# Kernel tuning notes

Hardware: AMD Instinct MI355X
Metric: run time of the kernel (lower is better)

The kernel has to match this reference:

```python
import jax, jax.numpy as jnp
import numpy as np

WINDOW = 512
STEP = WINDOW // 2


def hamming_window(n):
    # torch.hamming_window default is periodic=True: 0.54 - 0.46*cos(2*pi*k/n)
    return (0.54 - 0.46 * jnp.cos(2.0 * jnp.pi * jnp.arange(n) / n)).astype(jnp.float32)


def fft_convolve(a, b):
    # ortho-normalized rfft spectra, irfft, crop back to n samples.
    n = a.shape[-1]
    pa = jnp.pad(a, [(0, 0)] * (a.ndim - 1) + [(0, n)])
    pb = jnp.pad(b, [(0, 0)] * (b.ndim - 1) + [(0, n)])
    spec = jnp.fft.rfft(pa, axis=-1, norm='ortho') * jnp.fft.rfft(pb, axis=-1, norm='ortho')
    return jnp.fft.irfft(spec, n=2 * n, axis=-1, norm='ortho')[..., :n]


def fft_shift(a, shift):
    # repo's fft_shift: fractional shift via phase ramp in rfft domain of the
    n = a.shape[-1]
    shift_samples = shift * n * 0.5  # [..., 1]
    pa = jnp.pad(a, [(0, 0)] * (a.ndim - 1) + [(0, n)])
    spec = jnp.fft.rfft(pa, axis=-1, norm='ortho')  # [..., n+1]
    n_coeffs = spec.shape[-1]
    ramp = (jnp.arange(n_coeffs) * 2j * jnp.pi) / n_coeffs
    phase = jnp.exp(-ramp * shift_samples)  # broadcast over last dim
    return jnp.fft.irfft(spec * phase, n=2 * n, axis=-1, norm='ortho')


def setup_inputs() -> dict:
    key = jax.random.key(0)
    k1, k2 = jax.random.split(key)
    B, n = 4, 32768
    recon = jax.random.normal(k1, (B, 1, n), dtype=jnp.float32)
    target = jax.random.normal(k2, (B, 1, n), dtype=jnp.float32)
    return {"recon": recon, "target": target}


def reference(recon, target):
    batch = recon.shape[0]
    n_samples = recon.shape[-1]
    n_frames = (n_samples - WINDOW) // STEP + 1  # unfold(-1, 512, 256)

    # unfold: gather overlapping frames [B, n_frames, WINDOW]
    idx = jnp.arange(n_frames)[:, None] * STEP + jnp.arange(WINDOW)[None, :]
    frames = recon[:, 0, :][:, idx]  # [B, n_frames, WINDOW]
    windowed = (frames * hamming_window(WINDOW))[:, None, :, :]  # [B,1,F,W]

    # zero-pad each frame up to n_samples (the torch.cat with zeros)
    windowed = jnp.pad(windowed, ((0, 0), (0, 0), (0, 0), (0, n_samples - WINDOW)))

    # FFT cross-correlation surrogate against the full target
    fm = fft_convolve(windowed, target[:, :, None, :])[..., :n_samples]  # [B,1,F,n]

    positions = jnp.argmax(fm, axis=-1, keepdims=True).astype(jnp.float32) / n_samples

    positioned = fft_shift(windowed, positions)[..., :n_samples]  # [B,1,F,n]
    positioned = jnp.sum(positioned, axis=2).reshape(batch, 1, n_samples)

    return jnp.mean((positioned - target) ** 2)
```

## Files before the change

kernel.cpp:

```cpp
#include <hip/hip_runtime.h>
#include <math.h>

#define N_SAMP   32768
#define WINDOW   512
#define STEP     256
#define NFRAMES  127
#define NB       4
#define RTRUNC   1280
#define NSLAB    32
#define BPAD     776
#define HW       3104

#define WS_WF   0
#define WS_WFH  260096
#define WS_WFL  391168
#define WS_PV   522240
#define WS_M    587776
#define WS_CNT  588288
#define WS_LIST 588304
#define WS_H    592400
#define WS_PART 2169232

typedef _Float16 f16x8 __attribute__((ext_vector_type(8)));
typedef float f32x16 __attribute__((ext_vector_type(16)));

#define SW(L) ((L) ^ (((L) >> 3) & 7))

#define FMA4(A, LO, HI)                                           \
    A.x = fmaf(c.x, HI.x, A.x); A.x = fmaf(c.y, LO.w, A.x);       \
    A.x = fmaf(c.z, LO.z, A.x); A.x = fmaf(c.w, LO.y, A.x);       \
    A.y = fmaf(c.x, HI.y, A.y); A.y = fmaf(c.y, HI.x, A.y);       \
    A.y = fmaf(c.z, LO.w, A.y); A.y = fmaf(c.w, LO.z, A.y);       \
    A.z = fmaf(c.x, HI.z, A.z); A.z = fmaf(c.y, HI.y, A.z);       \
    A.z = fmaf(c.z, HI.x, A.z); A.z = fmaf(c.w, LO.w, A.z);       \
    A.w = fmaf(c.x, HI.w, A.w); A.w = fmaf(c.y, HI.z, A.w);       \
    A.w = fmaf(c.z, HI.y, A.w); A.w = fmaf(c.w, HI.x, A.w);

__global__ __launch_bounds__(256) void k_wf(const float* __restrict__ recon,
                                            float* __restrict__ wf,
                                            _Float16* __restrict__ wfh) {
    int e = blockIdx.x * 256 + threadIdx.x;
    int w     = e & 511;
    int bf128 = e >> 9;
    int f = bf128 & 127;
    int b = bf128 >> 7;
    float val = 0.f;
    if (f < NFRAMES) {
        float ham = 0.54f - 0.46f * (float)cos((double)w * (M_PI / 256.0));
        val = ham * recon[b * N_SAMP + f * STEP + w];
        wf[(b * NFRAMES + f) * 512 + w] = val;
    }
    size_t tr = (((size_t)b * 64 + (w >> 3)) * 128 + f) * 8 + (w & 7);
    wfh[tr] = (_Float16)val;
}

__global__ __launch_bounds__(256, 4) void k_argmax_mfma(
        const float* __restrict__ tgt,
        const _Float16* __restrict__ wfh,
        float* __restrict__ pv) {
    __shared__ _Float16 sbh[8 * BPAD];
    const int tid   = threadIdx.x;
    const int chunk = blockIdx.x & 127;
    const int half  = (blockIdx.x >> 7) & 1;
    const int b     = blockIdx.x >> 8;
    const int T0    = chunk * 256;
    const int TB    = T0 + 255;
    const float* tb = tgt + b * N_SAMP;

    for (int oc = tid; oc < 768; oc += 256) {
        int r = oc / 96, s = oc - r * 96;
        int base = TB - r - 8 * s;
        _Float16 h8[8];
#pragma unroll
        for (int j = 0; j < 8; ++j) {
            int t = base - j;
            h8[j] = (_Float16)((t >= 0) ? tb[t] : 0.0f);
        }
        *(f16x8*)&sbh[r * BPAD + 8 * s] = *(f16x8*)h8;
    }
    __syncthreads();

    const int wv  = tid >> 6;
    const int q   = (tid >> 5) & 1;
    const int cl  = tid & 31;
    const int nt0 = 2 * wv;
    const int rp  = 7 - (cl & 7);
    const _Float16* Ah0 = wfh + ((size_t)b * 64) * 1024 + (half * 64 + cl) * 8;

    f32x16 acc00 = (f32x16)(0.f);
    f32x16 acc01 = (f32x16)(0.f);
    f32x16 acc10 = (f32x16)(0.f);
    f32x16 acc11 = (f32x16)(0.f);

    int off = q * 1024;
    int ea  = rp * BPAD + (255 - 32 * nt0 - cl + 8 * q - rp);
    f16x8 a0  = *(const f16x8*)(Ah0 + off);
    f16x8 a1  = *(const f16x8*)(Ah0 + off + 256);
    f16x8 bh0 = *(const f16x8*)&sbh[ea];
    f16x8 bh1 = *(const f16x8*)&sbh[ea - 32];
#pragma unroll
    for (int k0 = 0; k0 < 512; k0 += 16) {
        f16x8 a0n  = *(const f16x8*)(Ah0 + off + 2048);
        f16x8 a1n  = *(const f16x8*)(Ah0 + off + 2304);
        f16x8 bh0n = *(const f16x8*)&sbh[ea + 16];
        f16x8 bh1n = *(const f16x8*)&sbh[ea - 16];
        acc00 = __builtin_amdgcn_mfma_f32_32x32x16_f16(a0, bh0, acc00, 0, 0, 0);
        acc01 = __builtin_amdgcn_mfma_f32_32x32x16_f16(a0, bh1, acc01, 0, 0, 0);
        acc10 = __builtin_amdgcn_mfma_f32_32x32x16_f16(a1, bh0, acc10, 0, 0, 0);
        acc11 = __builtin_amdgcn_mfma_f32_32x32x16_f16(a1, bh1, acc11, 0, 0, 0);
        a0 = a0n; a1 = a1n; bh0 = bh0n; bh1 = bh1n;
        off += 2048; ea += 16;
    }

    __syncthreads();
    float* sval = (float*)sbh;
#pragma unroll
    for (int r = 0; r < 16; ++r) {
        float v0 = fmaxf(acc00[r], acc01[r]);
        float v1 = fmaxf(acc10[r], acc11[r]);
#pragma unroll
        for (int mm = 1; mm <= 16; mm <<= 1) {
            v0 = fmaxf(v0, __shfl_xor(v0, mm));
            v1 = fmaxf(v1, __shfl_xor(v1, mm));
        }
        if (cl == 0) {
            int row = (r & 3) + 8 * (r >> 2) + 4 * q;
            sval[row * 4 + wv]        = v0;
            sval[(32 + row) * 4 + wv] = v1;
        }
    }
    __syncthreads();
    if (tid < 64) {
        float v = fmaxf(fmaxf(sval[tid * 4], sval[tid * 4 + 1]),
                        fmaxf(sval[tid * 4 + 2], sval[tid * 4 + 3]));
        pv[((size_t)b * 128 + half * 64 + tid) * 128 + chunk] = v;
    }
}

__global__ __launch_bounds__(256) void k_vmax(const float* __restrict__ tgt,
                                              const float* __restrict__ wf,
                                              const float* __restrict__ pv,
                                              int* __restrict__ marr) {
    __shared__ float wfr[512];
    __shared__ float tg[768];
    __shared__ float rv[256];
    __shared__ int   ri[256];
    __shared__ int   clist[32];
    __shared__ int   ccnt;
    const int tid = threadIdx.x;
    const int fr  = blockIdx.x;
    const int b   = fr / NFRAMES;
    const int f   = fr - b * NFRAMES;
    const float* prow = pv + ((size_t)b * 128 + f) * 128;
    const float* tb   = tgt + b * N_SAMP;

    for (int i = tid; i < 512; i += 256) wfr[i] = wf[(size_t)fr * 512 + i];

    float mv = (tid < 128) ? prow[tid] : -3.4e38f;
    rv[tid] = mv;
    __syncthreads();
    for (int s = 128; s > 0; s >>= 1) {
        if (tid < s) rv[tid] = fmaxf(rv[tid], rv[tid + s]);
        __syncthreads();
    }
    float m0 = rv[0];
    if (tid == 0) ccnt = 0;
    __syncthreads();
    float eps = 0.012f * fabsf(m0) + 1e-3f;
    if (tid < 128 && mv >= m0 - eps) {
        int k = atomicAdd(&ccnt, 1);
        if (k < 32) clist[k] = tid;
    }
    __syncthreads();
    int nc = ccnt;
    int total = (nc <= 32) ? nc : 128;
    float bestv = -3.4e38f; int bestt = 0x7fffffff;
    for (int ci = 0; ci < total; ++ci) {
        int c = (nc <= 32) ? clist[ci] : ci;
        int T0 = c * 256;
        __syncthreads();
        for (int y = tid; y < 768; y += 256) {
            int t = T0 - 511 + y;
            tg[y] = (t >= 0 && t < N_SAMP) ? tb[t] : 0.0f;
        }
        __syncthreads();
        float a = 0.f;
        for (int w2 = 0; w2 < 512; ++w2)
            a = fmaf(wfr[w2], tg[511 + tid - w2], a);
        int tt = T0 + tid;
        if (a > bestv || (a == bestv && tt < bestt)) { bestv = a; bestt = tt; }
    }
    rv[tid] = bestv; ri[tid] = bestt;
    __syncthreads();
    for (int s = 128; s > 0; s >>= 1) {
        if (tid < s) {
            float v2 = rv[tid + s]; int i2 = ri[tid + s];
            if (v2 > rv[tid] || (v2 == rv[tid] && i2 < ri[tid])) {
                rv[tid] = v2; ri[tid] = i2;
            }
        }
        __syncthreads();
    }
    if (tid == 0) marr[fr] = ri[0];
}

__global__ __launch_bounds__(256) void k_coef(const int* __restrict__ marr,
                                              float* __restrict__ hbuf) {
    const int bf  = blockIdx.x;
    const int tid = threadIdx.x;
    const double invD = 1.0 / 2147549184.0;
    const float  sd   = 4.7936899603827e-05f;
    const float  trf  = (float)(RTRUNC + 4) / 65536.0f;
    int m = marr[bf];
    int p = (int)rint((double)m * (32768.0 / 32769.0));
    int jlo = p - (RTRUNC + 8); if (jlo < -512) jlo = -512; jlo &= ~3;
    float* hr = hbuf + (size_t)bf * HW;
    if (m == 0) {
        for (int k4 = tid; k4 < 776; k4 += 256) {
            int j0 = jlo + 4 * k4;
            float4 vq = make_float4((j0 == 0) ? 1.0f : 0.0f, 0.f, 0.f, 0.f);
            *(float4*)(hr + 4 * k4) = vq;
        }
        return;
    }
    double md32768 = (double)m * 32768.0;
    double sp = sin((double)m * (M_PI / 32769.0));
    float Cp = (float)(sp * (1.0 / 65536.0));
    if (m & 1) Cp = -Cp;
    float Cn = -Cp;
    for (int k4 = tid; k4 < 776; k4 += 256) {
        int j0 = jlo + 4 * k4;
        double A0 = (double)j0 * 32769.0 - md32768;
        double rA0 = A0 * invD;
        float f0v = (float)(rA0 - rint(rA0));
        float4 vq;
        if (fabsf(f0v) > trf) {
            vq = make_float4(0.f, 0.f, 0.f, 0.f);
        } else if (fabsf(f0v) < 6.2e-5f) {
#pragma unroll
            for (int k = 0; k < 4; ++k) {
                double rA = (A0 + (double)k * 32769.0) * invD;
                float ff = (float)(rA - rint(rA));
                float r2;
                if (ff == 0.0f) r2 = 65535.0f;
                else {
                    float s, c2;
                    __sincosf((float)M_PI * ff, &s, &c2);
                    r2 = c2 * __builtin_amdgcn_rcpf(s);
                }
                ((float*)&vq)[k] = ((k & 1) ? Cn : Cp) * r2;
            }
        } else {
            float s, c2;
            __sincosf((float)M_PI * f0v, &s, &c2);
            vq.x = Cp * (c2 * __builtin_amdgcn_rcpf(s));
            float s1 = fmaf(c2, sd, s);
            float c1 = fmaf(-s, sd, c2);
            vq.y = Cn * (c1 * __builtin_amdgcn_rcpf(s1));
            float s2 = fmaf(c1, sd, s1);
            float cc2 = fmaf(-s1, sd, c1);
            vq.z = Cp * (cc2 * __builtin_amdgcn_rcpf(s2));
            float s3 = fmaf(cc2, sd, s2);
            float c3 = fmaf(-s2, sd, cc2);
            vq.w = Cn * (c3 * __builtin_amdgcn_rcpf(s3));
        }
        *(float4*)(hr + 4 * k4) = vq;
    }
}

__global__ __launch_bounds__(256) void k_sched(const int* __restrict__ marr,
                                               int* __restrict__ list,
                                               int* __restrict__ cnt,
                                               int nslab) {
    __shared__ int scnt[64];
    __shared__ int total;
    const int tid = threadIdx.x;
    if (tid < 64) scnt[tid] = 0;
    if (tid == 0) total = 0;
    __syncthreads();
    const int RT8 = RTRUNC + 8;
    for (int bf = tid; bf < NB * NFRAMES; bf += 256) {
        int b = bf / NFRAMES;
        int m = marr[bf];
        int p = (int)rint((double)m * (32768.0 / 32769.0));
        int lo = p - RT8;        if (lo < 0) lo = 0;
        int hi = p + RT8 + 511;  if (hi > N_SAMP - 1) hi = N_SAMP - 1;
        int r0 = lo >> 11, r1 = hi >> 11;
        for (int r = r0; r <= r1; ++r) {
            int bc = (b << 4) | r;
            int s = atomicAdd(&scnt[bc], 1);
            int k = atomicAdd(&total, 1);
            list[k] = (bf << 16) | (r << 8) | s;
        }
    }
    __syncthreads();
    int n = total;
    for (int k = tid; k < n; k += 256) {
        int v = list[k];
        int bf = (v >> 16) & 0x3fff;
        int r = (v >> 8) & 15;
        int b = bf / NFRAMES;
        if (scnt[(b << 4) | r] > nslab) list[k] = v | (1 << 30);
    }
    if (tid == 0) {
        int mx = 0;
        for (int i = 0; i < 64; ++i) mx = (scnt[i] > mx) ? scnt[i] : mx;
        cnt[0] = n;
        cnt[1] = (mx > nslab) ? nslab : mx;
    }
}

#define LDBLK2(nn) (*(const float4*)(s_h + 4 * SW(Lt + (nn))))
#define CB3(g, A, Bq, Cq)                                         \
    {                                                             \
        float4 tnew = LDBLK2(126 - (g));                          \
        const float4 c = wc[(g)];                                 \
        FMA4(acc0, w[A], w[Bq]); FMA4(acc1, w[Bq], w[Cq]);        \
        w[Cq] = tnew;                                             \
    }
#define CB3_NL(g, A, Bq, Cq)                                      \
    {                                                             \
        const float4 c = wc[(g)];                                 \
        FMA4(acc0, w[A], w[Bq]); FMA4(acc1, w[Bq], w[Cq]);        \
    }

__global__ __launch_bounds__(256, 8) void k_shift_acc(const float* __restrict__ wf,
                                                      const int* __restrict__ marr,
                                                      const int* __restrict__ list,
                                                      const int* __restrict__ cnt,
                                                      const float* __restrict__ hbuf,
                                                      float* __restrict__ part,
                                                      int slabmask) {
    __shared__ __align__(16) float s_h[2560];
    const int tid = threadIdx.x;
    const int Lt  = 2 * tid;
    const int Ltw = (tid >> 6) * 128;
    const int n   = cnt[0];

    for (int se = blockIdx.x; se < n; se += gridDim.x) {
        int v     = list[se];
        int bf    = (v >> 16) & 0x3fff;
        int r     = (v >> 8) & 15;
        int slot  = v & 255;
        int isat  = (v >> 30) & 1;
        int b     = bf / NFRAMES;
        int t0s   = r << 11;
        const float4* __restrict__ wc = (const float4*)(wf + bf * 512);

        int m  = marr[bf];
        int pr = (int)rint((double)m * (32768.0 / 32769.0));
        int jlo = pr - (RTRUNC + 8); if (jlo < -512) jlo = -512; jlo &= ~3;
        int kb0 = ((t0s - 512) - jlo) >> 2;
        const float4* __restrict__ hb = (const float4*)(hbuf + (size_t)bf * HW);

        __syncthreads();
        for (int e4 = tid; e4 < 640; e4 += 256) {
            int kb = kb0 + e4;
            float4 vq = (kb >= 0 && kb < 776) ? hb[kb]
                                              : make_float4(0.f, 0.f, 0.f, 0.f);
            *(float4*)(s_h + 4 * SW(e4)) = vq;
        }
        __syncthreads();

        int blo = (pr - (RTRUNC + 8) - (t0s - 512)) >> 2;
        int bhi = (pr + (RTRUNC + 8) - (t0s - 512)) >> 2;
        if (blo < 0) blo = 0;
        if (bhi > 639) bhi = 639;

        float4 acc0 = make_float4(0.f, 0.f, 0.f, 0.f);
        float4 acc1 = acc0;

        int gmin = Ltw + 127 - bhi; if (gmin < 0) gmin = 0;
        int gmax = Ltw + 255 - blo; if (gmax > 127) gmax = 127;
        if (gmin <= gmax) {
            int go0 = gmin / 3;
            bool tail = (gmax >= 126);
            int goE = tail ? 42 : (gmax / 3 + 1);
            int gb0 = 3 * go0;
            float4 w[3];
            w[0] = LDBLK2(127 - gb0);
            w[1] = LDBLK2(128 - gb0);
            w[2] = LDBLK2(129 - gb0);
            for (int go = go0; go < goE && go < 42; ++go) {
                const int gb = 3 * go;
                CB3(gb + 0, 0, 1, 2);
                CB3(gb + 1, 2, 0, 1);
                CB3(gb + 2, 1, 2, 0);
            }
            if (tail) { CB3(126, 0, 1, 2); CB3_NL(127, 2, 0, 1); }
        }

        int slab = slot & slabmask;
        float* ob = part + (size_t)slab * (NB * N_SAMP) + b * N_SAMP + t0s;
        if (!isat) {
            *(float4*)(ob + 8 * tid)     = acc0;
            *(float4*)(ob + 8 * tid + 4) = acc1;
        } else {
            float* p0 = ob + 8 * tid;
            atomicAdd(p0 + 0, acc0.x); atomicAdd(p0 + 1, acc0.y);
            atomicAdd(p0 + 2, acc0.z); atomicAdd(p0 + 3, acc0.w);
            atomicAdd(p0 + 4, acc1.x); atomicAdd(p0 + 5, acc1.y);
            atomicAdd(p0 + 6, acc1.z); atomicAdd(p0 + 7, acc1.w);
        }
    }
}

__global__ __launch_bounds__(256) void k_mse(const float* __restrict__ part,
                                             const float* __restrict__ tgt,
                                             float* __restrict__ out,
                                             const int* __restrict__ cnt,
                                             int nslab) {
    __shared__ float sred[4];
    int e = blockIdx.x * 256 + threadIdx.x;
    int ng = cnt[1];
    if (ng > nslab) ng = nslab;
    float s0 = 0.f, s1 = 0.f, s2 = 0.f, s3 = 0.f;
    int g = 0;
    for (; g + 4 <= ng; g += 4) {
        s0 += part[(size_t)(g + 0) * (NB * N_SAMP) + e];
        s1 += part[(size_t)(g + 1) * (NB * N_SAMP) + e];
        s2 += part[(size_t)(g + 2) * (NB * N_SAMP) + e];
        s3 += part[(size_t)(g + 3) * (NB * N_SAMP) + e];
    }
    for (; g < ng; ++g)
        s0 += part[(size_t)g * (NB * N_SAMP) + e];
    float s = (s0 + s1) + (s2 + s3);
    float d = s - tgt[e];
    float v = d * d;
#pragma unroll
    for (int off = 32; off > 0; off >>= 1) v += __shfl_down(v, off, 64);
    int lane = threadIdx.x & 63, wid = threadIdx.x >> 6;
    if (lane == 0) sred[wid] = v;
    __syncthreads();
    if (threadIdx.x == 0) {
        float sm = sred[0] + sred[1] + sred[2] + sred[3];
        atomicAdd(out, sm * (1.0f / 131072.0f));
    }
}

extern "C" void kernel_launch(void* const* d_in, const int* in_sizes, int n_in,
                              void* d_out, int out_size, void* d_ws, size_t ws_size,
                              hipStream_t stream) {
    const float* recon = (const float*)d_in[0];
    const float* tgt   = (const float*)d_in[1];
    float* out = (float*)d_out;
    float* W   = (float*)d_ws;

    float*     wf   = W + WS_WF;
    _Float16*  wfh  = (_Float16*)(W + WS_WFH);
    float*     pv   = W + WS_PV;
    int*       marr = (int*)(W + WS_M);
    int*       cnt  = (int*)(W + WS_CNT);
    int*       list = (int*)(W + WS_LIST);
    float*     hbuf = W + WS_H;
    float*     part = W + WS_PART;

    int nslab = NSLAB;
    while (nslab > 1 &&
           ((size_t)WS_PART + (size_t)nslab * NB * N_SAMP) * sizeof(float) > ws_size)
        nslab >>= 1;

    hipMemsetAsync(out, 0, sizeof(float), stream);
    hipMemsetAsync(part, 0, (size_t)nslab * NB * N_SAMP * sizeof(float), stream);

    k_wf<<<1024, 256, 0, stream>>>(recon, wf, wfh);
    k_argmax_mfma<<<1024, 256, 0, stream>>>(tgt, wfh, pv);
    k_vmax<<<NB * NFRAMES, 256, 0, stream>>>(tgt, wf, pv, marr);
    k_coef<<<NB * NFRAMES, 256, 0, stream>>>(marr, hbuf);
    k_sched<<<1, 256, 0, stream>>>(marr, list, cnt, nslab);
    k_shift_acc<<<2048, 256, 0, stream>>>(wf, marr, list, cnt, hbuf, part, nslab - 1);
    k_mse<<<512, 256, 0, stream>>>(part, tgt, out, cnt, nslab);
}
```

Before: 181.0 us.

## Split shift-accumulate work items in half and give each thread four outputs

Each scheduled 2048-sample segment becomes two 1024-sample half-segments, so every block handles half as much output and each thread produces four outputs instead of eight. The shared-memory staging buffer shrinks to match. The inner loop is rewritten as a two-step sliding window over float4 taps with a single accumulator, and the grid is doubled. The aim is more parallelism and occupancy with a smaller LDS footprint. The cost is that the coefficient and staging loads are repeated for each half, and each thread has less reuse of its loaded values.

```diff
diff --git a/kernel.cpp b/kernel.cpp
--- a/kernel.cpp
+++ b/kernel.cpp
@@ -310,19 +310,7 @@
     }
 }
 
-#define LDBLK2(nn) (*(const float4*)(s_h + 4 * SW(Lt + (nn))))
-#define CB3(g, A, Bq, Cq)                                         \
-    {                                                             \
-        float4 tnew = LDBLK2(126 - (g));                          \
-        const float4 c = wc[(g)];                                 \
-        FMA4(acc0, w[A], w[Bq]); FMA4(acc1, w[Bq], w[Cq]);        \
-        w[Cq] = tnew;                                             \
-    }
-#define CB3_NL(g, A, Bq, Cq)                                      \
-    {                                                             \
-        const float4 c = wc[(g)];                                 \
-        FMA4(acc0, w[A], w[Bq]); FMA4(acc1, w[Bq], w[Cq]);        \
-    }
+#define LDB(nn) (*(const float4*)(s_h + 4 * SW((nn) + 4)))
 
 __global__ __launch_bounds__(256, 8) void k_shift_acc(const float* __restrict__ wf,
                                                       const int* __restrict__ marr,
@@ -331,76 +319,72 @@
                                                       const float* __restrict__ hbuf,
                                                       float* __restrict__ part,
                                                       int slabmask) {
-    __shared__ __align__(16) float s_h[2560];
+    __shared__ __align__(16) float s_h[4 * 392];
     const int tid = threadIdx.x;
-    const int Lt  = 2 * tid;
-    const int Ltw = (tid >> 6) * 128;
-    const int n   = cnt[0];
-
-    for (int se = blockIdx.x; se < n; se += gridDim.x) {
-        int v     = list[se];
+    const int Lh  = tid;
+    const int W0  = tid & ~63;
+    const int n2  = 2 * cnt[0];
+
+    for (int se = blockIdx.x; se < n2; se += gridDim.x) {
+        int v     = list[se >> 1];
+        int hh    = se & 1;
         int bf    = (v >> 16) & 0x3fff;
         int r     = (v >> 8) & 15;
         int slot  = v & 255;
         int isat  = (v >> 30) & 1;
         int b     = bf / NFRAMES;
-        int t0s   = r << 11;
-        const float4* __restrict__ wc = (const float4*)(wf + bf * 512);
+        int t0h   = (r << 11) + (hh << 10);
 
         int m  = marr[bf];
         int pr = (int)rint((double)m * (32768.0 / 32769.0));
         int jlo = pr - (RTRUNC + 8); if (jlo < -512) jlo = -512; jlo &= ~3;
-        int kb0 = ((t0s - 512) - jlo) >> 2;
+        int kb0 = ((t0h - 512) - jlo) >> 2;
         const float4* __restrict__ hb = (const float4*)(hbuf + (size_t)bf * HW);
-
-        __syncthreads();
-        for (int e4 = tid; e4 < 640; e4 += 256) {
-            int kb = kb0 + e4;
+        const float4* __restrict__ wc = (const float4*)(wf + bf * 512);
+
+        __syncthreads();
+        for (int e4 = tid; e4 < 388; e4 += 256) {
+            int kb = kb0 + e4 - 4;
             float4 vq = (kb >= 0 && kb < 776) ? hb[kb]
                                               : make_float4(0.f, 0.f, 0.f, 0.f);
             *(float4*)(s_h + 4 * SW(e4)) = vq;
         }
         __syncthreads();
 
-        int blo = (pr - (RTRUNC + 8) - (t0s - 512)) >> 2;
-        int bhi = (pr + (RTRUNC + 8) - (t0s - 512)) >> 2;
+        int blo = (pr - (RTRUNC + 8) - (t0h - 512)) >> 2;
+        int bhi = (pr + (RTRUNC + 8) - (t0h - 512)) >> 2;
         if (blo < 0) blo = 0;
-        if (bhi > 639) bhi = 639;
-
-        float4 acc0 = make_float4(0.f, 0.f, 0.f, 0.f);
-        float4 acc1 = acc0;
-
-        int gmin = Ltw + 127 - bhi; if (gmin < 0) gmin = 0;
-        int gmax = Ltw + 255 - blo; if (gmax > 127) gmax = 127;
+        if (bhi > 383) bhi = 383;
+
+        float4 acc = make_float4(0.f, 0.f, 0.f, 0.f);
+
+        int gmin = W0 + 127 - bhi; if (gmin < 0) gmin = 0;
+        int gmax = W0 + 191 - blo; if (gmax > 127) gmax = 127;
         if (gmin <= gmax) {
-            int go0 = gmin / 3;
-            bool tail = (gmax >= 126);
-            int goE = tail ? 42 : (gmax / 3 + 1);
-            int gb0 = 3 * go0;
-            float4 w[3];
-            w[0] = LDBLK2(127 - gb0);
-            w[1] = LDBLK2(128 - gb0);
-            w[2] = LDBLK2(129 - gb0);
-            for (int go = go0; go < goE && go < 42; ++go) {
-                const int gb = 3 * go;
-                CB3(gb + 0, 0, 1, 2);
-                CB3(gb + 1, 2, 0, 1);
-                CB3(gb + 2, 1, 2, 0);
+            int p0 = gmin & ~1;
+            float4 wA = LDB(Lh + 127 - p0);
+            float4 wB = LDB(Lh + 128 - p0);
+            float4 wC = LDB(Lh + 126 - p0);
+            float4 wD = LDB(Lh + 125 - p0);
+            for (int p = p0; p <= gmax; p += 2) {
+                float4 n1 = LDB(Lh + 124 - p);
+                float4 n2v = LDB(Lh + 123 - p);
+                { const float4 c = wc[p]; FMA4(acc, wA, wB); }
+                if (p + 1 <= 127) {
+                    const float4 c = wc[p + 1]; FMA4(acc, wC, wA);
+                }
+                wA = wD; wB = wC; wC = n1; wD = n2v;
             }
-            if (tail) { CB3(126, 0, 1, 2); CB3_NL(127, 2, 0, 1); }
         }
 
         int slab = slot & slabmask;
-        float* ob = part + (size_t)slab * (NB * N_SAMP) + b * N_SAMP + t0s;
+        float* ob = part + (size_t)slab * (NB * N_SAMP) + b * N_SAMP + t0h;
         if (!isat) {
-            *(float4*)(ob + 8 * tid)     = acc0;
-            *(float4*)(ob + 8 * tid + 4) = acc1;
+            *(float4*)(ob + 4 * tid) = acc;
         } else {
-            float* p0 = ob + 8 * tid;
-            atomicAdd(p0 + 0, acc0.x); atomicAdd(p0 + 1, acc0.y);
-            atomicAdd(p0 + 2, acc0.z); atomicAdd(p0 + 3, acc0.w);
-            atomicAdd(p0 + 4, acc1.x); atomicAdd(p0 + 5, acc1.y);
-            atomicAdd(p0 + 6, acc1.z); atomicAdd(p0 + 7, acc1.w);
+            float* p0f = ob + 4 * tid;
+            atomicAdd(p0f + 0, acc.x); atomicAdd(p0f + 1, acc.y);
+            atomicAdd(p0f + 2, acc.z); atomicAdd(p0f + 3, acc.w);
         }
     }
 }
@@ -468,6 +452,6 @@
     k_vmax<<<NB * NFRAMES, 256, 0, stream>>>(tgt, wf, pv, marr);
     k_coef<<<NB * NFRAMES, 256, 0, stream>>>(marr, hbuf);
     k_sched<<<1, 256, 0, stream>>>(marr, list, cnt, nslab);
-    k_shift_acc<<<2048, 256, 0, stream>>>(wf, marr, list, cnt, hbuf, part, nslab - 1);
+    k_shift_acc<<<4096, 256, 0, stream>>>(wf, marr, list, cnt, hbuf, part, nslab - 1);
     k_mse<<<512, 256, 0, stream>>>(part, tgt, out, cnt, nslab);
 }
```

Result: no change. 181.8 us (+0.4%).

## Split candidate chunks across wavefronts with register-blocked float4 correlation

Applied to the files above, without the earlier changes.

The exact-correlation refinement kernel now gives each wavefront its own candidate chunk and its own shared staging buffer. Each lane computes four consecutive lags using float4 register blocking, with window coefficients read directly from global memory. This removes the block-wide barriers per candidate and cuts shared-memory reads per FMA. The cost is uneven work across wavefronts when there are few candidates, and coefficient loads that now go through global/cache memory.

```diff
diff --git a/kernel.cpp b/kernel.cpp
--- a/kernel.cpp
+++ b/kernel.cpp
@@ -10,6 +10,7 @@
 #define NSLAB    32
 #define BPAD     776
 #define HW       3104
+#define VSTRIDE  193
 
 #define WS_WF   0
 #define WS_WFH  260096
@@ -141,20 +142,20 @@
                                               const float* __restrict__ wf,
                                               const float* __restrict__ pv,
                                               int* __restrict__ marr) {
-    __shared__ float wfr[512];
-    __shared__ float tg[768];
+    __shared__ __align__(16) float stg[4 * VSTRIDE * 4];
     __shared__ float rv[256];
     __shared__ int   ri[256];
     __shared__ int   clist[32];
     __shared__ int   ccnt;
-    const int tid = threadIdx.x;
-    const int fr  = blockIdx.x;
-    const int b   = fr / NFRAMES;
-    const int f   = fr - b * NFRAMES;
+    const int tid  = threadIdx.x;
+    const int lane = tid & 63;
+    const int wv   = tid >> 6;
+    const int fr   = blockIdx.x;
+    const int b    = fr / NFRAMES;
+    const int f    = fr - b * NFRAMES;
     const float* prow = pv + ((size_t)b * 128 + f) * 128;
     const float* tb   = tgt + b * N_SAMP;
-
-    for (int i = tid; i < 512; i += 256) wfr[i] = wf[(size_t)fr * 512 + i];
+    const float4* wcg = (const float4*)(wf + (size_t)fr * 512);
 
     float mv = (tid < 128) ? prow[tid] : -3.4e38f;
     rv[tid] = mv;
@@ -175,20 +176,35 @@
     int nc = ccnt;
     int total = (nc <= 32) ? nc : 128;
     float bestv = -3.4e38f; int bestt = 0x7fffffff;
-    for (int ci = 0; ci < total; ++ci) {
-        int c = (nc <= 32) ? clist[ci] : ci;
-        int T0 = c * 256;
-        __syncthreads();
-        for (int y = tid; y < 768; y += 256) {
-            int t = T0 - 511 + y;
-            tg[y] = (t >= 0 && t < N_SAMP) ? tb[t] : 0.0f;
-        }
-        __syncthreads();
-        float a = 0.f;
-        for (int w2 = 0; w2 < 512; ++w2)
-            a = fmaf(wfr[w2], tg[511 + tid - w2], a);
-        int tt = T0 + tid;
-        if (a > bestv || (a == bestv && tt < bestt)) { bestv = a; bestt = tt; }
+    float* myg = stg + wv * (VSTRIDE * 4);
+
+    for (int ci = wv; ci < total; ci += 4) {
+        int c2 = (nc <= 32) ? clist[ci] : ci;
+        int T0 = c2 * 256;
+        for (int e = lane; e < 192; e += 64) {
+            int A = T0 - 512 + 4 * e;
+            float4 vq = (A >= 0 && A < N_SAMP) ? *(const float4*)(tb + A)
+                                               : make_float4(0.f, 0.f, 0.f, 0.f);
+            *(float4*)(myg + 4 * e) = vq;
+        }
+        float4 acc = make_float4(0.f, 0.f, 0.f, 0.f);
+        float4 lo = *(const float4*)(myg + 4 * (lane + 127));
+        float4 hi = *(const float4*)(myg + 4 * (lane + 128));
+        for (int g = 0; g < 127; ++g) {
+            float4 nl = *(const float4*)(myg + 4 * (lane + 126 - g));
+            const float4 c = wcg[g];
+            FMA4(acc, lo, hi);
+            hi = lo; lo = nl;
+        }
+        {
+            const float4 c = wcg[127];
+            FMA4(acc, lo, hi);
+        }
+        int tt = T0 + 4 * lane;
+        if (acc.x > bestv || (acc.x == bestv && tt     < bestt)) { bestv = acc.x; bestt = tt;     }
+        if (acc.y > bestv || (acc.y == bestv && tt + 1 < bestt)) { bestv = acc.y; bestt = tt + 1; }
+        if (acc.z > bestv || (acc.z == bestv && tt + 2 < bestt)) { bestv = acc.z; bestt = tt + 2; }
+        if (acc.w > bestv || (acc.w == bestv && tt + 3 < bestt)) { bestv = acc.w; bestt = tt + 3; }
     }
     rv[tid] = bestv; ri[tid] = bestt;
     __syncthreads();
```

New measurement: 174.7 us. -3.5%, faster.
